# Kernel optimization log

Measured on AMD Instinct MI355X. Metric: run time of the kernel, lower is better.

## Reference

```python
import jax, jax.numpy as jnp
import numpy as np

N = 50000      # nodes
E = 800000     # edges (before self loops)
F_IN = 128
HID = 32
HEADS = 4
C = 64         # num_classes
SLOPE = 0.2    # LeakyReLU negative slope (PyG GATConv default)


def setup_inputs() -> dict:
    key = jax.random.key(0)
    ks = jax.random.split(key, 16)
    def nrm(k, shape, scale=0.1):
        return jax.random.normal(k, shape, jnp.float32) * scale
    x = jax.random.normal(ks[0], (N, F_IN), jnp.float32)
    edge_index = jax.random.randint(ks[1], (2, E), 0, N, jnp.int32)
    # layer 1: F_IN -> HID per head, concat -> HEADS*HID
    w1 = nrm(ks[2], (F_IN, HEADS * HID)); as1 = nrm(ks[3], (HEADS, HID)); ad1 = nrm(ks[4], (HEADS, HID)); b1 = nrm(ks[5], (HEADS * HID,))
    # layer 2: HEADS*HID -> HID per head, concat
    w2 = nrm(ks[6], (HEADS * HID, HEADS * HID)); as2 = nrm(ks[7], (HEADS, HID)); ad2 = nrm(ks[8], (HEADS, HID)); b2 = nrm(ks[9], (HEADS * HID,))
    # layer 3: HEADS*HID -> C, single head, no concat (mean)
    w3 = nrm(ks[10], (HEADS * HID, C)); as3 = nrm(ks[11], (1, C)); ad3 = nrm(ks[12], (1, C)); b3 = nrm(ks[13], (C,))
    return {"x": x, "edge_index": edge_index,
            "w1": w1, "as1": as1, "ad1": ad1, "b1": b1,
            "w2": w2, "as2": as2, "ad2": ad2, "b2": b2,
            "w3": w3, "as3": as3, "ad3": ad3, "b3": b3}


def gat_conv(x, src, dst, W, a_src, a_dst, bias, heads, oc, concat):
    n = x.shape[0]
    h = (x @ W).reshape(n, heads, oc)                       # [N,H,F]
    al_s = jnp.einsum('nhf,hf->nh', h, a_src)               # [N,H]
    al_d = jnp.einsum('nhf,hf->nh', h, a_dst)
    e = jax.nn.leaky_relu(al_s[src] + al_d[dst], SLOPE)     # [E,H]
    # segment softmax over incoming edges per destination node
    m = jax.ops.segment_max(e, dst, num_segments=n)
    e = jnp.exp(e - m[dst])
    denom = jax.ops.segment_sum(e, dst, num_segments=n)
    alpha = e / denom[dst]                                  # [E,H]
    out = jax.ops.segment_sum(h[src] * alpha[:, :, None], dst, num_segments=n)  # [N,H,F]
    out = out.reshape(n, heads * oc) if concat else out.mean(axis=1)
    return out + bias


def reference(x, edge_index, w1, as1, ad1, b1, w2, as2, ad2, b2, w3, as3, ad3, b3):
    n = x.shape[0]
    loops = jnp.arange(n, dtype=edge_index.dtype)
    src = jnp.concatenate([edge_index[0], loops])           # add self loops (PyG default)
    dst = jnp.concatenate([edge_index[1], loops])
    h = gat_conv(x, src, dst, w1, as1, ad1, b1, HEADS, HID, True)
    h = jax.nn.relu(h)                                      # dropout is identity in eval
    h = gat_conv(h, src, dst, w2, as2, ad2, b2, HEADS, HID, True)
    h = jax.nn.relu(h)
    h = gat_conv(h, src, dst, w3, as3, ad3, b3, 1, C, False)
    return jax.nn.log_softmax(h, axis=1)
```

## Files before the change

### kernel.cpp

```cpp
#include <hip/hip_runtime.h>
#include <hip/hip_bf16.h>
#include <math.h>

#define SLOPE 0.2f
typedef unsigned int uint_t;
typedef unsigned short ushort_t;

static __device__ __forceinline__ float lrelu(float v) { return v > 0.f ? v : SLOPE * v; }
static __device__ __forceinline__ ushort_t f2b(float f) {
  uint_t u = __float_as_uint(f);
  u += 0x7fffu + ((u >> 16) & 1u);
  return (ushort_t)(u >> 16);
}
static __device__ __forceinline__ float2 b2x2(uint_t u) {
  union { uint_t u; __hip_bfloat162 b; } cv;
  cv.u = u;
  return __bfloat1622float2(cv.b);
}


__device__ __forceinline__ void hist_body(const int* __restrict__ ei, int* __restrict__ ts,
                                          int E, int N, int NB, int NBUCK, int b) {
  __shared__ int h[256];
  int tid = threadIdx.x;
  h[tid] = 0;
  __syncthreads();
  int ET = E + N;
  int base = b * 4096;
#pragma unroll
  for (int j = 0; j < 16; ++j) {
    int i = base + j * 256 + tid;
    if (i < ET) {
      int d = (i < E) ? ei[E + i] : (i - E);
      atomicAdd(&h[d >> 8], 1);
    }
  }
  __syncthreads();
  if (tid < NBUCK) ts[tid * NB + b] = h[tid];
}

__global__ __launch_bounds__(256) void scan1(int* __restrict__ a, int* __restrict__ bsum, int L) {
  int tid = threadIdx.x;
  int base = blockIdx.x * 1024 + tid * 4;
  int c0 = (base + 0 < L) ? a[base + 0] : 0;
  int c1 = (base + 1 < L) ? a[base + 1] : 0;
  int c2 = (base + 2 < L) ? a[base + 2] : 0;
  int c3 = (base + 3 < L) ? a[base + 3] : 0;
  int s = c0 + c1 + c2 + c3;
  int lane = tid & 63, wid = tid >> 6;
  int pre = s;
#pragma unroll
  for (int off = 1; off < 64; off <<= 1) {
    int t = __shfl_up(pre, off);
    if (lane >= off) pre += t;
  }
  __shared__ int wsum[4];
  if (lane == 63) wsum[wid] = pre;
  __syncthreads();
  int woff = 0;
#pragma unroll
  for (int w = 0; w < 4; ++w) woff += (w < wid) ? wsum[w] : 0;
  int excl = woff + pre - s;
  if (base + 0 < L) a[base + 0] = excl;
  if (base + 1 < L) a[base + 1] = excl + c0;
  if (base + 2 < L) a[base + 2] = excl + c0 + c1;
  if (base + 3 < L) a[base + 3] = excl + c0 + c1 + c2;
  if (tid == 255) bsum[blockIdx.x] = wsum[0] + wsum[1] + wsum[2] + wsum[3];
}

__global__ __launch_bounds__(1024) void scan2(int* __restrict__ bsum, int nb) {
  __shared__ int sh[1024];
  int tid = threadIdx.x;
  int v = (tid < nb) ? bsum[tid] : 0;
  sh[tid] = v;
  __syncthreads();
  for (int off = 1; off < 1024; off <<= 1) {
    int add = (tid >= off) ? sh[tid - off] : 0;
    __syncthreads();
    sh[tid] += add;
    __syncthreads();
  }
  if (tid < nb) bsum[tid] = sh[tid] - v;
}

__device__ __forceinline__ void scan3_body(int* __restrict__ a, const int* __restrict__ bsum,
                                           int L, int b) {
  int tid = threadIdx.x;
  int base = b * 1024 + tid * 4;
  if (base >= L) return;
  int off = bsum[b];
#pragma unroll
  for (int j = 0; j < 4; ++j)
    if (base + j < L) a[base + j] += off;
}

__global__ __launch_bounds__(256) void part_kernel(const int* __restrict__ ei,
                                                   const int* __restrict__ ts,
                                                   uint_t* __restrict__ tmp,
                                                   int E, int N, int NB, int NBUCK) {
  __shared__ int bin[256];
  int tid = threadIdx.x, b = blockIdx.x;
  if (tid < NBUCK) bin[tid] = ts[tid * NB + b];
  __syncthreads();
  int ET = E + N;
  int base = b * 4096;
#pragma unroll
  for (int j = 0; j < 16; ++j) {
    int i = base + j * 256 + tid;
    if (i < ET) {
      int s, d;
      if (i < E) { s = ei[i]; d = ei[E + i]; } else { s = i - E; d = i - E; }
      int pos = atomicAdd(&bin[d >> 8], 1);
      tmp[pos] = ((uint_t)d << 16) | (uint_t)s;
    }
  }
}

__global__ __launch_bounds__(256) void bucket_kernel(const uint_t* __restrict__ tmp,
                                                     const int* __restrict__ ts,
                                                     int* __restrict__ rowptr,
                                                     int* __restrict__ esrc,
                                                     int N, int NB, int NBUCK, int ET) {
  __shared__ int h[256], pref[256], rank[256];
  __shared__ int wsum[4];
  int tid = threadIdx.x, d = blockIdx.x;
  int start = ts[d * NB];
  int end = (d == NBUCK - 1) ? ET : ts[(d + 1) * NB];
  h[tid] = 0; rank[tid] = 0;
  __syncthreads();
  for (int i = start + tid; i < end; i += 256)
    atomicAdd(&h[(tmp[i] >> 16) & 255], 1);
  __syncthreads();
  int v = h[tid];
  int lane = tid & 63, wid = tid >> 6;
  int inc = v;
#pragma unroll
  for (int off = 1; off < 64; off <<= 1) {
    int t = __shfl_up(inc, off);
    if (lane >= off) inc += t;
  }
  if (lane == 63) wsum[wid] = inc;
  __syncthreads();
  int woff = 0;
#pragma unroll
  for (int w = 0; w < 4; ++w) woff += (w < wid) ? wsum[w] : 0;
  pref[tid] = woff + inc - v;
  __syncthreads();
  int idx = d * 256 + tid;
  if (idx <= N) rowptr[idx] = start + pref[tid];
  for (int i = start + tid; i < end; i += 256) {
    uint_t v2 = tmp[i];
    int low = (v2 >> 16) & 255;
    int r = atomicAdd(&rank[low], 1);
    esrc[start + pref[low] + r] = (int)(v2 & 0xffffu);
  }
}


template<int OC, bool BF16IN>
__device__ __forceinline__ void gemm_body(const void* __restrict__ Xv,
                                          const float* __restrict__ W,
                                          ushort_t* __restrict__ H, int N, int bid) {
  const int K = 128;
  const int CT = OC / 4;
  const int RPT = 64 / (256 / CT);
  __shared__ float xs[K][68];
  int tid = threadIdx.x;
  long row0 = (long)bid * 64;
  if (BF16IN) {
    const ushort_t* X = (const ushort_t*)Xv;
#pragma unroll
    for (int i = 0; i < 4; ++i) {
      int flat = i * 256 + tid;
      int r = flat & 63, kc = flat >> 6;
      long row = row0 + r;
      long rr = row < N ? row : (long)(N - 1);
      uint4 v = *(const uint4*)(X + rr * K + kc * 8);
      uint_t vv[4] = {v.x, v.y, v.z, v.w};
#pragma unroll
      for (int j = 0; j < 4; ++j) {
        float2 f = b2x2(vv[j]);
        xs[kc * 8 + j * 2 + 0][r] = f.x;
        xs[kc * 8 + j * 2 + 1][r] = f.y;
      }
    }
  } else {
    const float* X = (const float*)Xv;
#pragma unroll
    for (int i = 0; i < 8; ++i) {
      int flat = i * 256 + tid;
      int r = flat & 63, kc = flat >> 6;
      long row = row0 + r;
      long rr = row < N ? row : (long)(N - 1);
      float4 xv = *(const float4*)(X + rr * K + kc * 4);
      xs[kc * 4 + 0][r] = xv.x;
      xs[kc * 4 + 1][r] = xv.y;
      xs[kc * 4 + 2][r] = xv.z;
      xs[kc * 4 + 3][r] = xv.w;
    }
  }
  __syncthreads();
  int ct = tid % CT;
  int rg = tid / CT;
  int c0 = ct * 4;
  int r0 = rg * RPT;
  float acc[RPT][4];
#pragma unroll
  for (int i = 0; i < RPT; ++i)
    for (int j = 0; j < 4; ++j) acc[i][j] = 0.f;
#pragma unroll 4
  for (int k = 0; k < K; ++k) {
    float4 wv = *(const float4*)(W + (long)k * OC + c0);
    const float4* xr = (const float4*)(&xs[k][r0]);
#pragma unroll
    for (int i4 = 0; i4 < RPT / 4; ++i4) {
      float4 xv = xr[i4];
      float xa[4] = {xv.x, xv.y, xv.z, xv.w};
#pragma unroll
      for (int j = 0; j < 4; ++j) {
        int i = i4 * 4 + j;
        acc[i][0] = fmaf(xa[j], wv.x, acc[i][0]);
        acc[i][1] = fmaf(xa[j], wv.y, acc[i][1]);
        acc[i][2] = fmaf(xa[j], wv.z, acc[i][2]);
        acc[i][3] = fmaf(xa[j], wv.w, acc[i][3]);
      }
    }
  }
#pragma unroll
  for (int i = 0; i < RPT; ++i) {
    long row = row0 + r0 + i;
    if (row < N) {
      ushort4 o = {f2b(acc[i][0]), f2b(acc[i][1]), f2b(acc[i][2]), f2b(acc[i][3])};
      *(ushort4*)(H + row * OC + c0) = o;
    }
  }
}

template<int OC, bool BF16IN>
__global__ __launch_bounds__(256) void gemm_tile(const void* __restrict__ Xv,
                                                 const float* __restrict__ W,
                                                 ushort_t* __restrict__ H, int N) {
  gemm_body<OC, BF16IN>(Xv, W, H, N, blockIdx.x);
}

__global__ __launch_bounds__(256) void k_gemm1_hist(const float* __restrict__ X,
    const float* __restrict__ W, ushort_t* __restrict__ H, int N,
    const int* __restrict__ ei, int* __restrict__ ts, int E, int NB, int NBUCK,
    int gemmBlocks) {
  int bid = blockIdx.x;
  if (bid < gemmBlocks) gemm_body<128, false>(X, W, H, N, bid);
  else hist_body(ei, ts, E, N, NB, NBUCK, bid - gemmBlocks);
}


__device__ __forceinline__ void al4_body(const ushort_t* __restrict__ h,
                                         const float* __restrict__ a_s,
                                         const float* __restrict__ a_d,
                                         float* __restrict__ als, float* __restrict__ ald,
                                         int N, int bid) {
  int tid = threadIdx.x;
  int n = bid * 16 + (tid >> 4);
  int sl = tid & 15, hd = sl >> 2;
  if (n >= N) return;
  uint4 v = *(const uint4*)(h + (long)n * 128 + sl * 8);
  uint_t vv[4] = {v.x, v.y, v.z, v.w};
  const float* sp = a_s + hd * 32 + (sl & 3) * 8;
  const float* dp = a_d + hd * 32 + (sl & 3) * 8;
  float vs = 0.f, vd = 0.f;
#pragma unroll
  for (int j = 0; j < 4; ++j) {
    float2 f = b2x2(vv[j]);
    vs = fmaf(f.x, sp[j * 2 + 0], vs); vs = fmaf(f.y, sp[j * 2 + 1], vs);
    vd = fmaf(f.x, dp[j * 2 + 0], vd); vd = fmaf(f.y, dp[j * 2 + 1], vd);
  }
#pragma unroll
  for (int off = 1; off <= 2; off <<= 1) {
    vs += __shfl_xor(vs, off);
    vd += __shfl_xor(vd, off);
  }
  if ((sl & 3) == 0) { als[(long)n * 4 + hd] = vs; ald[(long)n * 4 + hd] = vd; }
}

__global__ void al_kernel4(const ushort_t* __restrict__ h, const float* __restrict__ a_s,
                           const float* __restrict__ a_d, float* __restrict__ als,
                           float* __restrict__ ald, int N) {
  al4_body(h, a_s, a_d, als, ald, N, blockIdx.x);
}

__global__ __launch_bounds__(256) void k_scan3_al4(int* __restrict__ a,
    const int* __restrict__ bsum, int L, int scanBlocks,
    const ushort_t* __restrict__ h, const float* __restrict__ a_s,
    const float* __restrict__ a_d, float* __restrict__ als, float* __restrict__ ald, int N) {
  int bid = blockIdx.x;
  if (bid < scanBlocks) scan3_body(a, bsum, L, bid);
  else al4_body(h, a_s, a_d, als, ald, N, bid - scanBlocks);
}

__global__ void al_kernel1(const ushort_t* __restrict__ h, const float* __restrict__ a_s,
                           const float* __restrict__ a_d, float* __restrict__ als,
                           float* __restrict__ ald, int N) {
  int tid = threadIdx.x;
  int n = blockIdx.x * 32 + (tid >> 3);
  int sl = tid & 7;
  if (n >= N) return;
  uint4 v = *(const uint4*)(h + (long)n * 64 + sl * 8);
  uint_t vv[4] = {v.x, v.y, v.z, v.w};
  const float* sp = a_s + sl * 8;
  const float* dp = a_d + sl * 8;
  float vs = 0.f, vd = 0.f;
#pragma unroll
  for (int j = 0; j < 4; ++j) {
    float2 f = b2x2(vv[j]);
    vs = fmaf(f.x, sp[j * 2 + 0], vs); vs = fmaf(f.y, sp[j * 2 + 1], vs);
    vd = fmaf(f.x, dp[j * 2 + 0], vd); vd = fmaf(f.y, dp[j * 2 + 1], vd);
  }
#pragma unroll
  for (int off = 1; off <= 4; off <<= 1) {
    vs += __shfl_xor(vs, off);
    vd += __shfl_xor(vd, off);
  }
  if (sl == 0) { als[n] = vs; ald[n] = vd; }
}


__global__ __launch_bounds__(256) void gat_agg128(const ushort_t* __restrict__ h,
    const float* __restrict__ als, const float* __restrict__ ald,
    const int* __restrict__ rowptr, const int* __restrict__ esrc,
    const float* __restrict__ bias, ushort_t* __restrict__ out, int N) {
  int tid = threadIdx.x;
  int n = blockIdx.x * 8 + (tid >> 5);
  int l = tid & 31;
  int slot = l >> 4, sl = l & 15, hd = sl >> 2;
  if (n >= N) return;
  int beg = rowptr[n], end = rowptr[n + 1];
  float aldv = ald[(long)n * 4 + hd];
  float den = 0.f;
  float acc[8] = {0.f, 0.f, 0.f, 0.f, 0.f, 0.f, 0.f, 0.f};
  for (int e = beg + slot; e < end; e += 2) {
    int s = esrc[e];
    float p = __expf(lrelu(als[(long)s * 4 + hd] + aldv));
    den += p;
    uint4 v = *(const uint4*)(h + (long)s * 128 + sl * 8);
    uint_t vv[4] = {v.x, v.y, v.z, v.w};
#pragma unroll
    for (int j = 0; j < 4; ++j) {
      float2 f = b2x2(vv[j]);
      acc[2 * j + 0] = fmaf(p, f.x, acc[2 * j + 0]);
      acc[2 * j + 1] = fmaf(p, f.y, acc[2 * j + 1]);
    }
  }
  den += __shfl_xor(den, 16);
#pragma unroll
  for (int j = 0; j < 8; ++j) acc[j] += __shfl_xor(acc[j], 16);
  if (slot == 0) {
    float inv = 1.f / den;
    float4 bv0 = *(const float4*)(bias + sl * 8);
    float4 bv1 = *(const float4*)(bias + sl * 8 + 4);
    float bb[8] = {bv0.x, bv0.y, bv0.z, bv0.w, bv1.x, bv1.y, bv1.z, bv1.w};
    uint_t pk[4];
#pragma unroll
    for (int j = 0; j < 4; ++j) {
      float v0 = fmaxf(fmaf(acc[2 * j + 0], inv, bb[2 * j + 0]), 0.f);
      float v1 = fmaxf(fmaf(acc[2 * j + 1], inv, bb[2 * j + 1]), 0.f);
      pk[j] = (uint_t)f2b(v0) | ((uint_t)f2b(v1) << 16);
    }
    uint4 pv = {pk[0], pk[1], pk[2], pk[3]};
    *(uint4*)(out + (long)n * 128 + sl * 8) = pv;
  }
}

__global__ __launch_bounds__(256) void gat_agg64_lsm(const ushort_t* __restrict__ h,
    const float* __restrict__ als, const float* __restrict__ ald,
    const int* __restrict__ rowptr, const int* __restrict__ esrc,
    const float* __restrict__ bias, float* __restrict__ out, int N) {
  int tid = threadIdx.x;
  int n = blockIdx.x * 8 + (tid >> 5);
  int l = tid & 31;
  int slot = l >> 3, sl = l & 7;
  if (n >= N) return;
  int beg = rowptr[n], end = rowptr[n + 1];
  float aldv = ald[n];
  float den = 0.f;
  float acc[8] = {0.f, 0.f, 0.f, 0.f, 0.f, 0.f, 0.f, 0.f};
  for (int e = beg + slot; e < end; e += 4) {
    int s = esrc[e];
    float p = __expf(lrelu(als[s] + aldv));
    den += p;
    uint4 v = *(const uint4*)(h + (long)s * 64 + sl * 8);
    uint_t vv[4] = {v.x, v.y, v.z, v.w};
#pragma unroll
    for (int j = 0; j < 4; ++j) {
      float2 f = b2x2(vv[j]);
      acc[2 * j + 0] = fmaf(p, f.x, acc[2 * j + 0]);
      acc[2 * j + 1] = fmaf(p, f.y, acc[2 * j + 1]);
    }
  }
  den += __shfl_xor(den, 8); den += __shfl_xor(den, 16);
#pragma unroll
  for (int j = 0; j < 8; ++j) {
    acc[j] += __shfl_xor(acc[j], 8);
    acc[j] += __shfl_xor(acc[j], 16);
  }
  if (slot == 0) {
    float inv = 1.f / den;
    float v[8];
#pragma unroll
    for (int j = 0; j < 8; ++j) v[j] = fmaf(acc[j], inv, bias[sl * 8 + j]);
    float lm = v[0];
#pragma unroll
    for (int j = 1; j < 8; ++j) lm = fmaxf(lm, v[j]);
#pragma unroll
    for (int off = 1; off <= 4; off <<= 1) lm = fmaxf(lm, __shfl_xor(lm, off));
    float es = 0.f;
#pragma unroll
    for (int j = 0; j < 8; ++j) es += __expf(v[j] - lm);
#pragma unroll
    for (int off = 1; off <= 4; off <<= 1) es += __shfl_xor(es, off);
    float lse = lm + __logf(es);
    float4 o0 = {v[0] - lse, v[1] - lse, v[2] - lse, v[3] - lse};
    float4 o1 = {v[4] - lse, v[5] - lse, v[6] - lse, v[7] - lse};
    *(float4*)(out + (long)n * 64 + sl * 8 + 0) = o0;
    *(float4*)(out + (long)n * 64 + sl * 8 + 4) = o1;
  }
}


extern "C" void kernel_launch(void* const* d_in, const int* in_sizes, int n_in,
                              void* d_out, int out_size, void* d_ws, size_t ws_size,
                              hipStream_t stream) {
  const float* x   = (const float*)d_in[0];
  const int*   ei  = (const int*)d_in[1];
  const float* w1  = (const float*)d_in[2];
  const float* as1 = (const float*)d_in[3];
  const float* ad1 = (const float*)d_in[4];
  const float* b1  = (const float*)d_in[5];
  const float* w2  = (const float*)d_in[6];
  const float* as2 = (const float*)d_in[7];
  const float* ad2 = (const float*)d_in[8];
  const float* b2  = (const float*)d_in[9];
  const float* w3  = (const float*)d_in[10];
  const float* as3 = (const float*)d_in[11];
  const float* ad3 = (const float*)d_in[12];
  const float* b3  = (const float*)d_in[13];
  float* out = (float*)d_out;

  const int N = in_sizes[0] / 128;
  const int E = in_sizes[1] / 2;
  const int ET = E + N;

  const int NB = (ET + 4095) / 4096;
  const int NBUCK = (N + 255) >> 8;
  const int SL = NBUCK * NB;
  const int nsb = (SL + 1023) / 1024;

  char* ws = (char*)d_ws;
  size_t off = 0;
  auto alloc = [&](size_t bytes) -> void* {
    void* p = ws + off;
    off += (bytes + 255) & ~(size_t)255;
    return p;
  };
  ushort_t* bufA = (ushort_t*)alloc((size_t)N * 128 * 2);
  ushort_t* bufB = (ushort_t*)alloc((size_t)N * 128 * 2);
  float* als   = (float*)alloc((size_t)N * 4 * 4);
  float* ald   = (float*)alloc((size_t)N * 4 * 4);
  int* ts      = (int*)alloc((size_t)SL * 4);
  int* bsum    = (int*)alloc((size_t)1024 * 4);
  uint_t* tmp  = (uint_t*)alloc((size_t)ET * 4);
  int* rowptr  = (int*)alloc((size_t)(N + 1) * 4);
  int* esrc    = (int*)alloc((size_t)ET * 4);

  const int ggrid = (N + 63) / 64;
  const int albk = (N + 15) / 16;
  const int aggrid = (N + 7) / 8;

  k_gemm1_hist<<<ggrid + NB, 256, 0, stream>>>(x, w1, bufA, N, ei, ts, E, NB, NBUCK, ggrid);
  scan1<<<nsb, 256, 0, stream>>>(ts, bsum, SL);
  scan2<<<1, 1024, 0, stream>>>(bsum, nsb);
  k_scan3_al4<<<nsb + albk, 256, 0, stream>>>(ts, bsum, SL, nsb,
                                              bufA, as1, ad1, als, ald, N);
  part_kernel<<<NB, 256, 0, stream>>>(ei, ts, tmp, E, N, NB, NBUCK);
  bucket_kernel<<<NBUCK, 256, 0, stream>>>(tmp, ts, rowptr, esrc, N, NB, NBUCK, ET);

  gat_agg128<<<aggrid, 256, 0, stream>>>(bufA, als, ald, rowptr, esrc, b1, bufB, N);

  gemm_tile<128, true><<<ggrid, 256, 0, stream>>>(bufB, w2, bufA, N);
  al_kernel4<<<albk, 256, 0, stream>>>(bufA, as2, ad2, als, ald, N);
  gat_agg128<<<aggrid, 256, 0, stream>>>(bufA, als, ald, rowptr, esrc, b2, bufB, N);

  gemm_tile<64, true><<<ggrid, 256, 0, stream>>>(bufB, w3, bufA, N);
  al_kernel1<<<(N + 31) / 32, 256, 0, stream>>>(bufA, as3, ad3, als, ald, N);
  gat_agg64_lsm<<<aggrid, 256, 0, stream>>>(bufA, als, ald, rowptr, esrc, b3, out, N);
}
```

Measured before the change: 315.7 us.

## Fuse attention-logit dot products into GEMM epilogue and drop scan3 pass

The per-node attention logits (als/ald) are now computed from the fp32 GEMM accumulators in the epilogue of each GEMM, using shuffle reductions across the column threads of a head. This removes the separate al_kernel4/al_kernel1 launches and their re-read of the bf16 features. The third scan pass is also removed: part_kernel and bucket_kernel add the block offset from bsum when they read the prefix sums. Logits now come from unrounded fp32 values rather than the bf16-rounded features, which shifts the numerics slightly, and the shuffle grouping depends on how threads map to columns.

```diff
diff --git a/kernel.cpp b/kernel.cpp
--- a/kernel.cpp
+++ b/kernel.cpp
@@ -83,24 +83,18 @@
   if (tid < nb) bsum[tid] = sh[tid] - v;
 }
 
-__device__ __forceinline__ void scan3_body(int* __restrict__ a, const int* __restrict__ bsum,
-                                           int L, int b) {
-  int tid = threadIdx.x;
-  int base = b * 1024 + tid * 4;
-  if (base >= L) return;
-  int off = bsum[b];
-#pragma unroll
-  for (int j = 0; j < 4; ++j)
-    if (base + j < L) a[base + j] += off;
-}
 
 __global__ __launch_bounds__(256) void part_kernel(const int* __restrict__ ei,
                                                    const int* __restrict__ ts,
+                                                   const int* __restrict__ bsum,
                                                    uint_t* __restrict__ tmp,
                                                    int E, int N, int NB, int NBUCK) {
   __shared__ int bin[256];
   int tid = threadIdx.x, b = blockIdx.x;
-  if (tid < NBUCK) bin[tid] = ts[tid * NB + b];
+  if (tid < NBUCK) {
+    int idx = tid * NB + b;
+    bin[tid] = ts[idx] + bsum[idx >> 10];
+  }
   __syncthreads();
   int ET = E + N;
   int base = b * 4096;
@@ -118,14 +112,20 @@
 
 __global__ __launch_bounds__(256) void bucket_kernel(const uint_t* __restrict__ tmp,
                                                      const int* __restrict__ ts,
+                                                     const int* __restrict__ bsum,
                                                      int* __restrict__ rowptr,
                                                      int* __restrict__ esrc,
                                                      int N, int NB, int NBUCK, int ET) {
   __shared__ int h[256], pref[256], rank[256];
   __shared__ int wsum[4];
   int tid = threadIdx.x, d = blockIdx.x;
-  int start = ts[d * NB];
-  int end = (d == NBUCK - 1) ? ET : ts[(d + 1) * NB];
+  int i0 = d * NB;
+  int start = ts[i0] + bsum[i0 >> 10];
+  int end = ET;
+  if (d != NBUCK - 1) {
+    int i1 = (d + 1) * NB;
+    end = ts[i1] + bsum[i1 >> 10];
+  }
   h[tid] = 0; rank[tid] = 0;
   __syncthreads();
   for (int i = start + tid; i < end; i += 256)
@@ -160,7 +160,12 @@
 template<int OC, bool BF16IN>
 __device__ __forceinline__ void gemm_body(const void* __restrict__ Xv,
                                           const float* __restrict__ W,
-                                          ushort_t* __restrict__ H, int N, int bid) {
+                                          ushort_t* __restrict__ H,
+                                          const float* __restrict__ a_s,
+                                          const float* __restrict__ a_d,
+                                          float* __restrict__ als,
+                                          float* __restrict__ ald,
+                                          int N, int bid) {
   const int K = 128;
   const int CT = OC / 4;
   const int RPT = 64 / (256 / CT);
@@ -234,92 +239,53 @@
       *(ushort4*)(H + row * OC + c0) = o;
     }
   }
+  float4 sv = *(const float4*)(a_s + c0);
+  float4 dv = *(const float4*)(a_d + c0);
+  const int RED = (OC == 128) ? 4 : 8;
+  const int GM  = (OC == 128) ? 7 : 15;
+#pragma unroll
+  for (int i = 0; i < RPT; ++i) {
+    float ps = acc[i][0] * sv.x + acc[i][1] * sv.y + acc[i][2] * sv.z + acc[i][3] * sv.w;
+    float pd = acc[i][0] * dv.x + acc[i][1] * dv.y + acc[i][2] * dv.z + acc[i][3] * dv.w;
+#pragma unroll
+    for (int off = 1; off <= RED; off <<= 1) {
+      ps += __shfl_xor(ps, off);
+      pd += __shfl_xor(pd, off);
+    }
+    long row = row0 + r0 + i;
+    if ((ct & GM) == 0 && row < N) {
+      if (OC == 128) {
+        int head = c0 >> 5;
+        als[row * 4 + head] = ps;
+        ald[row * 4 + head] = pd;
+      } else {
+        als[row] = ps;
+        ald[row] = pd;
+      }
+    }
+  }
 }
 
 template<int OC, bool BF16IN>
 __global__ __launch_bounds__(256) void gemm_tile(const void* __restrict__ Xv,
                                                  const float* __restrict__ W,
-                                                 ushort_t* __restrict__ H, int N) {
-  gemm_body<OC, BF16IN>(Xv, W, H, N, blockIdx.x);
+                                                 ushort_t* __restrict__ H,
+                                                 const float* __restrict__ a_s,
+                                                 const float* __restrict__ a_d,
+                                                 float* __restrict__ als,
+                                                 float* __restrict__ ald, int N) {
+  gemm_body<OC, BF16IN>(Xv, W, H, a_s, a_d, als, ald, N, blockIdx.x);
 }
 
 __global__ __launch_bounds__(256) void k_gemm1_hist(const float* __restrict__ X,
-    const float* __restrict__ W, ushort_t* __restrict__ H, int N,
+    const float* __restrict__ W, ushort_t* __restrict__ H,
+    const float* __restrict__ a_s, const float* __restrict__ a_d,
+    float* __restrict__ als, float* __restrict__ ald, int N,
     const int* __restrict__ ei, int* __restrict__ ts, int E, int NB, int NBUCK,
     int gemmBlocks) {
   int bid = blockIdx.x;
-  if (bid < gemmBlocks) gemm_body<128, false>(X, W, H, N, bid);
+  if (bid < gemmBlocks) gemm_body<128, false>(X, W, H, a_s, a_d, als, ald, N, bid);
   else hist_body(ei, ts, E, N, NB, NBUCK, bid - gemmBlocks);
-}
-
-
-__device__ __forceinline__ void al4_body(const ushort_t* __restrict__ h,
-                                         const float* __restrict__ a_s,
-                                         const float* __restrict__ a_d,
-                                         float* __restrict__ als, float* __restrict__ ald,
-                                         int N, int bid) {
-  int tid = threadIdx.x;
-  int n = bid * 16 + (tid >> 4);
-  int sl = tid & 15, hd = sl >> 2;
-  if (n >= N) return;
-  uint4 v = *(const uint4*)(h + (long)n * 128 + sl * 8);
-  uint_t vv[4] = {v.x, v.y, v.z, v.w};
-  const float* sp = a_s + hd * 32 + (sl & 3) * 8;
-  const float* dp = a_d + hd * 32 + (sl & 3) * 8;
-  float vs = 0.f, vd = 0.f;
-#pragma unroll
-  for (int j = 0; j < 4; ++j) {
-    float2 f = b2x2(vv[j]);
-    vs = fmaf(f.x, sp[j * 2 + 0], vs); vs = fmaf(f.y, sp[j * 2 + 1], vs);
-    vd = fmaf(f.x, dp[j * 2 + 0], vd); vd = fmaf(f.y, dp[j * 2 + 1], vd);
-  }
-#pragma unroll
-  for (int off = 1; off <= 2; off <<= 1) {
-    vs += __shfl_xor(vs, off);
-    vd += __shfl_xor(vd, off);
-  }
-  if ((sl & 3) == 0) { als[(long)n * 4 + hd] = vs; ald[(long)n * 4 + hd] = vd; }
-}
-
-__global__ void al_kernel4(const ushort_t* __restrict__ h, const float* __restrict__ a_s,
-                           const float* __restrict__ a_d, float* __restrict__ als,
-                           float* __restrict__ ald, int N) {
-  al4_body(h, a_s, a_d, als, ald, N, blockIdx.x);
-}
-
-__global__ __launch_bounds__(256) void k_scan3_al4(int* __restrict__ a,
-    const int* __restrict__ bsum, int L, int scanBlocks,
-    const ushort_t* __restrict__ h, const float* __restrict__ a_s,
-    const float* __restrict__ a_d, float* __restrict__ als, float* __restrict__ ald, int N) {
-  int bid = blockIdx.x;
-  if (bid < scanBlocks) scan3_body(a, bsum, L, bid);
-  else al4_body(h, a_s, a_d, als, ald, N, bid - scanBlocks);
-}
-
-__global__ void al_kernel1(const ushort_t* __restrict__ h, const float* __restrict__ a_s,
-                           const float* __restrict__ a_d, float* __restrict__ als,
-                           float* __restrict__ ald, int N) {
-  int tid = threadIdx.x;
-  int n = blockIdx.x * 32 + (tid >> 3);
-  int sl = tid & 7;
-  if (n >= N) return;
-  uint4 v = *(const uint4*)(h + (long)n * 64 + sl * 8);
-  uint_t vv[4] = {v.x, v.y, v.z, v.w};
-  const float* sp = a_s + sl * 8;
-  const float* dp = a_d + sl * 8;
-  float vs = 0.f, vd = 0.f;
-#pragma unroll
-  for (int j = 0; j < 4; ++j) {
-    float2 f = b2x2(vv[j]);
-    vs = fmaf(f.x, sp[j * 2 + 0], vs); vs = fmaf(f.y, sp[j * 2 + 1], vs);
-    vd = fmaf(f.x, dp[j * 2 + 0], vd); vd = fmaf(f.y, dp[j * 2 + 1], vd);
-  }
-#pragma unroll
-  for (int off = 1; off <= 4; off <<= 1) {
-    vs += __shfl_xor(vs, off);
-    vd += __shfl_xor(vd, off);
-  }
-  if (sl == 0) { als[n] = vs; ald[n] = vd; }
 }
 
 
@@ -471,24 +437,20 @@
   int* esrc    = (int*)alloc((size_t)ET * 4);
 
   const int ggrid = (N + 63) / 64;
-  const int albk = (N + 15) / 16;
   const int aggrid = (N + 7) / 8;
 
-  k_gemm1_hist<<<ggrid + NB, 256, 0, stream>>>(x, w1, bufA, N, ei, ts, E, NB, NBUCK, ggrid);
+  k_gemm1_hist<<<ggrid + NB, 256, 0, stream>>>(x, w1, bufA, as1, ad1, als, ald, N,
+                                               ei, ts, E, NB, NBUCK, ggrid);
   scan1<<<nsb, 256, 0, stream>>>(ts, bsum, SL);
   scan2<<<1, 1024, 0, stream>>>(bsum, nsb);
-  k_scan3_al4<<<nsb + albk, 256, 0, stream>>>(ts, bsum, SL, nsb,
-                                              bufA, as1, ad1, als, ald, N);
-  part_kernel<<<NB, 256, 0, stream>>>(ei, ts, tmp, E, N, NB, NBUCK);
-  bucket_kernel<<<NBUCK, 256, 0, stream>>>(tmp, ts, rowptr, esrc, N, NB, NBUCK, ET);
+  part_kernel<<<NB, 256, 0, stream>>>(ei, ts, bsum, tmp, E, N, NB, NBUCK);
+  bucket_kernel<<<NBUCK, 256, 0, stream>>>(tmp, ts, bsum, rowptr, esrc, N, NB, NBUCK, ET);
 
   gat_agg128<<<aggrid, 256, 0, stream>>>(bufA, als, ald, rowptr, esrc, b1, bufB, N);
 
-  gemm_tile<128, true><<<ggrid, 256, 0, stream>>>(bufB, w2, bufA, N);
-  al_kernel4<<<albk, 256, 0, stream>>>(bufA, as2, ad2, als, ald, N);
+  gemm_tile<128, true><<<ggrid, 256, 0, stream>>>(bufB, w2, bufA, as2, ad2, als, ald, N);
   gat_agg128<<<aggrid, 256, 0, stream>>>(bufA, als, ald, rowptr, esrc, b2, bufB, N);
 
-  gemm_tile<64, true><<<ggrid, 256, 0, stream>>>(bufB, w3, bufA, N);
-  al_kernel1<<<(N + 31) / 32, 256, 0, stream>>>(bufA, as3, ad3, als, ald, N);
+  gemm_tile<64, true><<<ggrid, 256, 0, stream>>>(bufB, w3, bufA, as3, ad3, als, ald, N);
   gat_agg64_lsm<<<aggrid, 256, 0, stream>>>(bufA, als, ald, rowptr, esrc, b3, out, N);
 }
```

Result: faster. 308.5 us (-2.3%).
